# Performance work log

Hardware: AMD Instinct MI355X
Metric: run time of the kernel (lower is better)

The kernel has to match this reference:

```python
import jax, jax.numpy as jnp
import numpy as np

N_HEAD = 16


def setup_inputs() -> dict:
    key = jax.random.key(0)
    ks = jax.random.split(key, 6)
    B, T, H = 4, 2048, 1024
    inp = jax.random.normal(ks[0], (B, T, H), dtype=jnp.float32)
    # padding mask: valid prefix of random length in [T//2, T] per batch row
    lengths = jax.random.randint(ks[1], (B, 1), T // 2, T + 1)
    mask = jnp.arange(T)[None, :] < lengths  # (B, T) bool
    s = 0.02
    w_qkv = jax.random.normal(ks[2], (H, 3 * H), dtype=jnp.float32) * s
    b_qkv = jax.random.normal(ks[3], (3 * H,), dtype=jnp.float32) * s
    w_out = jax.random.normal(ks[4], (H, H), dtype=jnp.float32) * s
    b_out = jax.random.normal(ks[5], (H,), dtype=jnp.float32) * s
    return {"input": inp, "mask": mask, "w_qkv": w_qkv, "b_qkv": b_qkv,
            "w_out": w_out, "b_out": b_out}


def reference(input, mask, w_qkv, b_qkv, w_out, b_out):
    B, T, H = input.shape
    hd = H // N_HEAD
    qkv = input @ w_qkv + b_qkv                       # (B, T, 3H)
    q, k, v = jnp.split(qkv, 3, axis=-1)
    # (B, T, H) -> (B, nh, T, hd)
    q = q.reshape(B, T, N_HEAD, hd).transpose(0, 2, 1, 3)
    k = k.reshape(B, T, N_HEAD, hd).transpose(0, 2, 1, 3)
    v = v.reshape(B, T, N_HEAD, hd).transpose(0, 2, 1, 3)
    scores = jnp.einsum('bhqd,bhkd->bhqk', q, k) / jnp.sqrt(jnp.float32(hd))
    causal = jnp.tril(jnp.ones((T, T), dtype=bool))   # (T, T)
    full_mask = causal[None, None, :, :] & mask[:, None, None, :]  # (B,1,T,T) bcast over heads
    scores = jnp.where(full_mask, scores, -jnp.inf)
    attn = jax.nn.softmax(scores, axis=-1)            # (B, nh, T, T)
    o = jnp.einsum('bhqk,bhkd->bhqd', attn, v)        # (B, nh, T, hd)
    o = o.transpose(0, 2, 1, 3).reshape(B, T, H)
    return o @ w_out + b_out
```

## Files before the change

### kernel.cpp

```cpp
#include <hip/hip_runtime.h>
#include <math.h>

#define B_  4
#define T_  2048
#define H_  1024
#define NH  16
#define HD  64
#define H3  3072

typedef short bf16x8 __attribute__((ext_vector_type(8)));
typedef short bf16x4 __attribute__((ext_vector_type(4)));
typedef float f32x4  __attribute__((ext_vector_type(4)));
typedef float f32x16 __attribute__((ext_vector_type(16)));

#define SC2F 0.18033688011112042f

__device__ __forceinline__ unsigned short f2bf(float f) {
    union { float f; unsigned u; } v; v.f = f;
    unsigned u = v.u;
    unsigned r = (u + 0x7fffu + ((u >> 16) & 1u)) >> 16;
    return (unsigned short)r;
}

__device__ __forceinline__ void gload_lds16(const void* g, void* l) {
    __builtin_amdgcn_global_load_lds(
        (const __attribute__((address_space(1))) unsigned*)g,
        (__attribute__((address_space(3))) unsigned*)l, 16, 0, 0);
}

__device__ __forceinline__ f32x4 mfma_16x16x16_bf16(bf16x4 a, bf16x4 b, f32x4 c) {
#if __has_builtin(__builtin_amdgcn_mfma_f32_16x16x16_bf16)
    return __builtin_amdgcn_mfma_f32_16x16x16_bf16(a, b, c, 0, 0, 0);
#elif __has_builtin(__builtin_amdgcn_mfma_f32_16x16x16bf16_1k)
    return __builtin_amdgcn_mfma_f32_16x16x16bf16_1k(a, b, c, 0, 0, 0);
#else
    f32x4 d;
    asm volatile("v_mfma_f32_16x16x16_bf16 %0, %1, %2, %3"
                 : "=v"(d) : "v"(a), "v"(b), "v"(c));
    return d;
#endif
}

__global__ void lengths_kernel(const void* mask, int* lengths) {
    int b = blockIdx.x;
    int t = threadIdx.x;
    const unsigned* mu = (const unsigned*)mask;
    bool is_byte = (mu[0] == 0x01010101u);
    int cnt = 0;
    if (is_byte) {
        const unsigned char* m8 = (const unsigned char*)mask;
        for (int i = t; i < T_; i += 256) cnt += (m8[b * T_ + i] != 0);
    } else {
        const unsigned* m32 = (const unsigned*)mask;
        for (int i = t; i < T_; i += 256) cnt += (m32[b * T_ + i] != 0);
    }
    __shared__ int red[256];
    red[t] = cnt;
    __syncthreads();
    for (int s = 128; s > 0; s >>= 1) {
        if (t < s) red[t] += red[t + s];
        __syncthreads();
    }
    if (t == 0) lengths[b] = red[0];
}

__global__ void convert_bf16_kernel(const float* __restrict__ x,
                                    unsigned short* __restrict__ y, int n) {
    int i = (blockIdx.x * 256 + threadIdx.x) * 4;
    if (i < n) {
        float4 v = *(const float4*)(x + i);
        ushort4 o;
        o.x = f2bf(v.x); o.y = f2bf(v.y); o.z = f2bf(v.z); o.w = f2bf(v.w);
        *(ushort4*)(y + i) = o;
    }
}

__global__ void transpose2_kernel(const float* __restrict__ Wqkv,
                                  unsigned short* __restrict__ WqkvT,
                                  const float* __restrict__ Wout,
                                  unsigned short* __restrict__ WoutT) {
    __shared__ unsigned short tile[32][33];
    const int K = H_;
    const float* in;
    unsigned short* out;
    int N, nb;
    if (blockIdx.x < 96) { in = Wqkv; out = WqkvT; N = H3; nb = blockIdx.x * 32; }
    else                 { in = Wout; out = WoutT; N = H_; nb = (blockIdx.x - 96) * 32; }
    int kb = blockIdx.y * 32;
    int tx = threadIdx.x, ty = threadIdx.y;
    for (int i = 0; i < 32; i += 8)
        tile[ty + i][tx] = f2bf(in[(long)(kb + ty + i) * N + nb + tx]);
    __syncthreads();
    for (int i = 0; i < 32; i += 8)
        out[(long)(nb + ty + i) * K + kb + tx] = tile[tx][ty + i];
}

template <bool BF16_OUT, bool KSCALE, bool VSPLIT>
__global__ __launch_bounds__(256) void gemm_kernel(
    const unsigned short* __restrict__ A,
    const unsigned short* __restrict__ Bt,
    const float* __restrict__ bias,
    void* __restrict__ C,
    unsigned short* __restrict__ Vt,
    int M, int N, int K)
{
    __shared__ unsigned short Asm[128][32];
    __shared__ unsigned short Bsm[128][32];

    int tn = blockIdx.x * 128, tm = blockIdx.y * 128;
    int tid = threadIdx.x;
    int wid = tid >> 6, lane = tid & 63;
    int l31 = lane & 31, lh = lane >> 5;
    int wm = (wid & 1) * 64, wn = (wid >> 1) * 64;
    int grow = lane >> 2;
    int gcol = (((lane & 3) ^ (grow & 3) ^ ((grow >> 2) & 3))) * 8;
    int rkey = (l31 & 3) ^ ((l31 >> 2) & 3);

    f32x16 acc[2][2] = {};

    for (int k0 = 0; k0 < K; k0 += 32) {
        __syncthreads();
#pragma unroll
        for (int t = 0; t < 2; t++) {
            int ar = wid * 32 + t * 16 + grow;
            gload_lds16(A  + (long)(tm + ar) * K + k0 + gcol, &Asm[wid * 32 + t * 16][0]);
            gload_lds16(Bt + (long)(tn + ar) * K + k0 + gcol, &Bsm[wid * 32 + t * 16][0]);
        }
        __syncthreads();

        bf16x8 af[2][2], bfv[2][2];
#pragma unroll
        for (int ks = 0; ks < 2; ks++) {
            int pc = ((2 * ks + lh) ^ rkey) * 8;
            af[ks][0]  = *(const bf16x8*)(&Asm[wm + l31][pc]);
            af[ks][1]  = *(const bf16x8*)(&Asm[wm + 32 + l31][pc]);
            bfv[ks][0] = *(const bf16x8*)(&Bsm[wn + l31][pc]);
            bfv[ks][1] = *(const bf16x8*)(&Bsm[wn + 32 + l31][pc]);
        }
#pragma unroll
        for (int ks = 0; ks < 2; ks++)
#pragma unroll
            for (int i = 0; i < 2; i++)
#pragma unroll
                for (int j = 0; j < 2; j++)
                    acc[i][j] = __builtin_amdgcn_mfma_f32_32x32x16_bf16(
                        af[ks][i], bfv[ks][j], acc[i][j], 0, 0, 0);
    }

    if (VSPLIT && tn >= 2 * H_) {
#pragma unroll
        for (int i = 0; i < 2; i++)
#pragma unroll
            for (int j = 0; j < 2; j++) {
                int col = tn + wn + j * 32 + l31;
                float bs = bias[col];
                int feat = col - 2 * H_;
#pragma unroll
                for (int rg = 0; rg < 4; rg++) {
                    int tok0 = tm + wm + i * 32 + rg * 8 + lh * 4;
                    int bb = tok0 >> 11;
                    unsigned d0 = (unsigned)f2bf(acc[i][j][rg * 4 + 0] + bs) |
                                  ((unsigned)f2bf(acc[i][j][rg * 4 + 1] + bs) << 16);
                    unsigned d1 = (unsigned)f2bf(acc[i][j][rg * 4 + 2] + bs) |
                                  ((unsigned)f2bf(acc[i][j][rg * 4 + 3] + bs) << 16);
                    unsigned short* dst = Vt + ((long)(bb * 1024 + feat)) * T_ + (tok0 & (T_ - 1));
                    *(uint2*)dst = make_uint2(d0, d1);
                }
            }
        return;
    }

#pragma unroll
    for (int i = 0; i < 2; i++)
#pragma unroll
        for (int j = 0; j < 2; j++) {
            int col = tn + wn + j * 32 + l31;
            float bs = bias[col];
            bool ks_ = KSCALE && (col >= H_) && (col < 2 * H_);
#pragma unroll
            for (int r = 0; r < 16; r++) {
                int row = tm + wm + i * 32 + (r & 3) + 8 * (r >> 2) + 4 * lh;
                float v = acc[i][j][r] + bs;
                if (ks_) v *= SC2F;
                if (BF16_OUT)
                    ((unsigned short*)C)[(long)row * N + col] = f2bf(v);
                else
                    ((float*)C)[(long)row * N + col] = v;
            }
        }
}

__global__ __launch_bounds__(256) void attn_kernel(
    const unsigned short* __restrict__ QKV,
    const unsigned short* __restrict__ Vt,
    const int* __restrict__ lengths,
    unsigned short* __restrict__ O)
{
    int idx = blockIdx.x;
    int bh = idx & 63;
    int qt = 15 - (idx >> 6);
    int b = bh >> 4, h = bh & 15;
    int len = lengths[b];
    int q0 = qt * 128;

    int tid = threadIdx.x;
    int wid = tid >> 6, lane = tid & 63, quad = lane >> 4, lr = lane & 15;

    __shared__ __align__(16) unsigned short SH[18432];
    unsigned short (*Kd)[64][72] = (unsigned short (*)[64][72])(&SH[0]);
    unsigned short (*Vd)[64][72] = (unsigned short (*)[64][72])(&SH[9216]);

    const long qkv_base = (long)b * T_ * H3;

    bf16x8 qf[2][2];
#pragma unroll
    for (int nq = 0; nq < 2; nq++)
#pragma unroll
        for (int ks = 0; ks < 2; ks++)
            qf[nq][ks] = *(const bf16x8*)(QKV + qkv_base +
                (long)(q0 + wid * 32 + nq * 16 + lr) * H3 + h * HD + ks * 32 + quad * 8);

    int srow = tid >> 2, scb = (tid & 3) * 16;
    const unsigned short* kbase = QKV + qkv_base + (long)srow * H3 + H_ + h * HD + scb;
    const unsigned short* vbase = Vt + ((long)(bh * 64 + srow)) * T_ + scb;

    {
        float4 k0 = *(const float4*)(kbase);
        float4 k1 = *(const float4*)(kbase + 8);
        float4 v0 = *(const float4*)(vbase);
        float4 v1 = *(const float4*)(vbase + 8);
        *(float4*)(&Kd[0][srow][scb])     = k0;
        *(float4*)(&Kd[0][srow][scb + 8]) = k1;
        *(float4*)(&Vd[0][srow][scb])     = v0;
        *(float4*)(&Vd[0][srow][scb + 8]) = v1;
    }
    __syncthreads();

    float l_i[2] = { 0.f, 0.f };
    f32x4 Oacc[4][2] = {};

    int kmax = min(q0 + 127, len - 1);
    int n_kt = (kmax >> 6) + 1;
    int q_wave_lo = q0 + wid * 32;
    int q_wave_hi = q_wave_lo + 31;
    int myq[2] = { q_wave_lo + lr, q_wave_lo + 16 + lr };

    const unsigned short* kp = kbase + (long)64 * H3;
    const unsigned short* vp = vbase + 64;

    for (int kt = 0; kt < n_kt; kt++) {
        int cur = kt & 1;
        float4 pk0, pk1, pv0, pv1;
        bool pf = (kt + 1 < n_kt);
        if (pf) {
            pk0 = *(const float4*)(kp);
            pk1 = *(const float4*)(kp + 8);
            pv0 = *(const float4*)(vp);
            pv1 = *(const float4*)(vp + 8);
            kp += (long)64 * H3;
            vp += 64;
        }

        int k_lo = kt * 64;
        if (!(k_lo > q_wave_hi || k_lo >= len)) {
            f32x4 Sacc[4][2] = {};
#pragma unroll
            for (int ks = 0; ks < 2; ks++) {
#pragma unroll
                for (int mt = 0; mt < 4; mt++) {
                    bf16x8 kf = *(const bf16x8*)(&Kd[cur][mt * 16 + lr][ks * 32 + quad * 8]);
                    Sacc[mt][0] = __builtin_amdgcn_mfma_f32_16x16x32_bf16(kf, qf[0][ks], Sacc[mt][0], 0, 0, 0);
                    Sacc[mt][1] = __builtin_amdgcn_mfma_f32_16x16x32_bf16(kf, qf[1][ks], Sacc[mt][1], 0, 0, 0);
                }
            }

            bool full = (k_lo + 63 <= q_wave_lo) && (k_lo + 63 < len);
            float rs[2] = { 0.f, 0.f };
            unsigned pkk[4][2][2];
#pragma unroll
            for (int mt = 0; mt < 4; mt++)
#pragma unroll
                for (int nq = 0; nq < 2; nq++) {
                    float p[4];
#pragma unroll
                    for (int r = 0; r < 4; r++) {
                        float s = Sacc[mt][nq][r];
                        if (!full) {
                            int key = k_lo + mt * 16 + quad * 4 + r;
                            bool ok = (key <= myq[nq]) && (key < len);
                            s = ok ? s : -INFINITY;
                        }
                        p[r] = __builtin_amdgcn_exp2f(s);
                        rs[nq] += p[r];
                    }
                    pkk[mt][nq][0] = __builtin_amdgcn_perm(__float_as_uint(p[1]), __float_as_uint(p[0]), 0x07060302);
                    pkk[mt][nq][1] = __builtin_amdgcn_perm(__float_as_uint(p[3]), __float_as_uint(p[2]), 0x07060302);
                }

#pragma unroll
            for (int nq = 0; nq < 2; nq++) {
                float v = rs[nq];
                v += __shfl_xor(v, 16);
                v += __shfl_xor(v, 32);
                l_i[nq] += v;
            }

#pragma unroll
            for (int mt = 0; mt < 4; mt++) {
                union { unsigned u[2]; bf16x4 v; } bu[2];
                bu[0].u[0] = pkk[mt][0][0]; bu[0].u[1] = pkk[mt][0][1];
                bu[1].u[0] = pkk[mt][1][0]; bu[1].u[1] = pkk[mt][1][1];
#pragma unroll
                for (int md = 0; md < 4; md++) {
                    bf16x4 vf = *(const bf16x4*)(&Vd[cur][md * 16 + lr][mt * 16 + quad * 4]);
                    Oacc[md][0] = mfma_16x16x16_bf16(vf, bu[0].v, Oacc[md][0]);
                    Oacc[md][1] = mfma_16x16x16_bf16(vf, bu[1].v, Oacc[md][1]);
                }
            }
        }

        if (pf) {
            *(float4*)(&Kd[cur ^ 1][srow][scb])     = pk0;
            *(float4*)(&Kd[cur ^ 1][srow][scb + 8]) = pk1;
            *(float4*)(&Vd[cur ^ 1][srow][scb])     = pv0;
            *(float4*)(&Vd[cur ^ 1][srow][scb + 8]) = pv1;
        }
        __syncthreads();
    }

    __syncthreads();
    {
        unsigned short (*Es)[68] = (unsigned short (*)[68])(&SH[0]);
        float inv[2] = { 1.f / l_i[0], 1.f / l_i[1] };
#pragma unroll
        for (int nq = 0; nq < 2; nq++)
#pragma unroll
            for (int md = 0; md < 4; md++)
#pragma unroll
                for (int rp = 0; rp < 2; rp++) {
                    float e0 = Oacc[md][nq][rp * 2]     * inv[nq];
                    float e1 = Oacc[md][nq][rp * 2 + 1] * inv[nq];
                    unsigned w = __builtin_amdgcn_perm(__float_as_uint(e1), __float_as_uint(e0), 0x07060302);
                    *(unsigned*)(&Es[wid * 32 + nq * 16 + lr][md * 16 + quad * 4 + rp * 2]) = w;
                }
        __asm__ volatile("s_waitcnt lgkmcnt(0)" ::: "memory");
        int row = lane >> 1, cb = (lane & 1) * 32;
        long tok = (long)b * T_ + q0 + wid * 32 + row;
#pragma unroll
        for (int i = 0; i < 4; i++) {
            float4 v = *(const float4*)(&Es[wid * 32 + row][cb + i * 8]);
            *(float4*)(&O[tok * H_ + h * HD + cb + i * 8]) = v;
        }
    }
}

extern "C" void kernel_launch(void* const* d_in, const int* in_sizes, int n_in,
                              void* d_out, int out_size, void* d_ws, size_t ws_size,
                              hipStream_t stream) {
    const float* X    = (const float*)d_in[0];
    const void*  mask = d_in[1];
    const float* Wqkv = (const float*)d_in[2];
    const float* bqkv = (const float*)d_in[3];
    const float* Wout = (const float*)d_in[4];
    const float* bout = (const float*)d_in[5];

    char* ws = (char*)d_ws;
    int* lengths          = (int*)ws;
    unsigned short* WqkvT = (unsigned short*)(ws + 256);
    unsigned short* WoutT = WqkvT + (long)H3 * H_;
    unsigned short* QKV   = WoutT + (long)H_ * H_;
    unsigned short* Xbf   = QKV + (long)B_ * T_ * H3;
    unsigned short* Vt    = Xbf + (long)B_ * T_ * H_;
    unsigned short* Obf   = Xbf;

    const int M = B_ * T_;

    lengths_kernel<<<B_, 256, 0, stream>>>(mask, lengths);
    convert_bf16_kernel<<<(M * H_ / 4 + 255) / 256, 256, 0, stream>>>(X, Xbf, M * H_);
    transpose2_kernel<<<dim3(128, H_ / 32), dim3(32, 8), 0, stream>>>(Wqkv, WqkvT, Wout, WoutT);
    gemm_kernel<true, true, true><<<dim3(H3 / 128, M / 128), 256, 0, stream>>>(
        Xbf, WqkvT, bqkv, QKV, Vt, M, H3, H_);
    attn_kernel<<<B_ * NH * (T_ / 128), 256, 0, stream>>>(QKV, Vt, lengths, Obf);
    gemm_kernel<false, false, false><<<dim3(H_ / 128, M / 128), 256, 0, stream>>>(
        Obf, WoutT, bout, d_out, nullptr, M, H_, H_);
}
```

Measured before the change: 287.6 us.

## Use direct global-to-LDS loads in attention and deepen GEMM K-tile

The attention kernel now stages K and V tiles with direct global-to-LDS async loads into an XOR-swizzled unpadded layout, instead of register prefetch followed by LDS stores. This removes VGPR staging and the padding. The GEMM K step doubles to 64 with a new swizzle, and it gains a TN template parameter so the output projection uses 64-wide N tiles and launches twice as many blocks. The cost is more LDS per GEMM block and a sync placement that now depends on the async load ordering.

```diff
diff --git a/kernel.cpp b/kernel.cpp
--- a/kernel.cpp
+++ b/kernel.cpp
@@ -95,7 +95,7 @@
         out[(long)(nb + ty + i) * K + kb + tx] = tile[tx][ty + i];
 }
 
-template <bool BF16_OUT, bool KSCALE, bool VSPLIT>
+template <int TN, bool BF16_OUT, bool KSCALE, bool VSPLIT>
 __global__ __launch_bounds__(256) void gemm_kernel(
     const unsigned short* __restrict__ A,
     const unsigned short* __restrict__ Bt,
@@ -104,54 +104,56 @@
     unsigned short* __restrict__ Vt,
     int M, int N, int K)
 {
-    __shared__ unsigned short Asm[128][32];
-    __shared__ unsigned short Bsm[128][32];
-
-    int tn = blockIdx.x * 128, tm = blockIdx.y * 128;
+    __shared__ unsigned short Asm[128][64];
+    __shared__ unsigned short Bsm[TN][64];
+
+    int tn = blockIdx.x * TN, tm = blockIdx.y * 128;
     int tid = threadIdx.x;
     int wid = tid >> 6, lane = tid & 63;
     int l31 = lane & 31, lh = lane >> 5;
-    int wm = (wid & 1) * 64, wn = (wid >> 1) * 64;
-    int grow = lane >> 2;
-    int gcol = (((lane & 3) ^ (grow & 3) ^ ((grow >> 2) & 3))) * 8;
-    int rkey = (l31 & 3) ^ ((l31 >> 2) & 3);
-
-    f32x16 acc[2][2] = {};
-
-    for (int k0 = 0; k0 < K; k0 += 32) {
+    int wm = (wid & 1) * 64, wn = (wid >> 1) * (TN / 2);
+
+    int rl = lane >> 3;
+    int g8 = ((lane & 7) ^ rl) * 8;
+    const unsigned short* aP = A  + (long)(tm + wid * 32 + rl) * K + g8;
+    const unsigned short* bP = Bt + (long)(tn + wid * (TN / 4) + rl) * K + g8;
+    int rk = l31 & 7;
+
+    f32x16 acc[2][TN / 64] = {};
+
+    for (int k0 = 0; k0 < K; k0 += 64) {
         __syncthreads();
 #pragma unroll
-        for (int t = 0; t < 2; t++) {
-            int ar = wid * 32 + t * 16 + grow;
-            gload_lds16(A  + (long)(tm + ar) * K + k0 + gcol, &Asm[wid * 32 + t * 16][0]);
-            gload_lds16(Bt + (long)(tn + ar) * K + k0 + gcol, &Bsm[wid * 32 + t * 16][0]);
-        }
+        for (int t = 0; t < 4; t++)
+            gload_lds16(aP + (long)(t * 8) * K + k0, &Asm[wid * 32 + t * 8][0]);
+#pragma unroll
+        for (int t = 0; t < TN / 32; t++)
+            gload_lds16(bP + (long)(t * 8) * K + k0, &Bsm[wid * (TN / 4) + t * 8][0]);
         __syncthreads();
 
-        bf16x8 af[2][2], bfv[2][2];
-#pragma unroll
-        for (int ks = 0; ks < 2; ks++) {
-            int pc = ((2 * ks + lh) ^ rkey) * 8;
-            af[ks][0]  = *(const bf16x8*)(&Asm[wm + l31][pc]);
-            af[ks][1]  = *(const bf16x8*)(&Asm[wm + 32 + l31][pc]);
-            bfv[ks][0] = *(const bf16x8*)(&Bsm[wn + l31][pc]);
-            bfv[ks][1] = *(const bf16x8*)(&Bsm[wn + 32 + l31][pc]);
-        }
-#pragma unroll
-        for (int ks = 0; ks < 2; ks++)
+#pragma unroll
+        for (int ks = 0; ks < 4; ks++) {
+            int pc = ((ks * 2 + lh) ^ rk) * 8;
+            bf16x8 af[2], bv[TN / 64];
+            af[0] = *(const bf16x8*)(&Asm[wm + l31][pc]);
+            af[1] = *(const bf16x8*)(&Asm[wm + 32 + l31][pc]);
+#pragma unroll
+            for (int j = 0; j < TN / 64; j++)
+                bv[j] = *(const bf16x8*)(&Bsm[wn + j * 32 + l31][pc]);
 #pragma unroll
             for (int i = 0; i < 2; i++)
 #pragma unroll
-                for (int j = 0; j < 2; j++)
+                for (int j = 0; j < TN / 64; j++)
                     acc[i][j] = __builtin_amdgcn_mfma_f32_32x32x16_bf16(
-                        af[ks][i], bfv[ks][j], acc[i][j], 0, 0, 0);
+                        af[i], bv[j], acc[i][j], 0, 0, 0);
+        }
     }
 
     if (VSPLIT && tn >= 2 * H_) {
 #pragma unroll
         for (int i = 0; i < 2; i++)
 #pragma unroll
-            for (int j = 0; j < 2; j++) {
+            for (int j = 0; j < TN / 64; j++) {
                 int col = tn + wn + j * 32 + l31;
                 float bs = bias[col];
                 int feat = col - 2 * H_;
@@ -173,7 +175,7 @@
 #pragma unroll
     for (int i = 0; i < 2; i++)
 #pragma unroll
-        for (int j = 0; j < 2; j++) {
+        for (int j = 0; j < TN / 64; j++) {
             int col = tn + wn + j * 32 + l31;
             float bs = bias[col];
             bool ks_ = KSCALE && (col >= H_) && (col < 2 * H_);
@@ -206,9 +208,9 @@
     int tid = threadIdx.x;
     int wid = tid >> 6, lane = tid & 63, quad = lane >> 4, lr = lane & 15;
 
-    __shared__ __align__(16) unsigned short SH[18432];
-    unsigned short (*Kd)[64][72] = (unsigned short (*)[64][72])(&SH[0]);
-    unsigned short (*Vd)[64][72] = (unsigned short (*)[64][72])(&SH[9216]);
+    __shared__ __align__(16) unsigned short SH[16384];
+    unsigned short (*Kd)[64][64] = (unsigned short (*)[64][64])(&SH[0]);
+    unsigned short (*Vd)[64][64] = (unsigned short (*)[64][64])(&SH[8192]);
 
     const long qkv_base = (long)b * T_ * H3;
 
@@ -220,21 +222,10 @@
             qf[nq][ks] = *(const bf16x8*)(QKV + qkv_base +
                 (long)(q0 + wid * 32 + nq * 16 + lr) * H3 + h * HD + ks * 32 + quad * 8);
 
-    int srow = tid >> 2, scb = (tid & 3) * 16;
-    const unsigned short* kbase = QKV + qkv_base + (long)srow * H3 + H_ + h * HD + scb;
-    const unsigned short* vbase = Vt + ((long)(bh * 64 + srow)) * T_ + scb;
-
-    {
-        float4 k0 = *(const float4*)(kbase);
-        float4 k1 = *(const float4*)(kbase + 8);
-        float4 v0 = *(const float4*)(vbase);
-        float4 v1 = *(const float4*)(vbase + 8);
-        *(float4*)(&Kd[0][srow][scb])     = k0;
-        *(float4*)(&Kd[0][srow][scb + 8]) = k1;
-        *(float4*)(&Vd[0][srow][scb])     = v0;
-        *(float4*)(&Vd[0][srow][scb + 8]) = v1;
-    }
-    __syncthreads();
+    int rl = lane >> 3;
+    int g8 = ((lane & 7) ^ rl) * 8;
+    const unsigned short* kB = QKV + qkv_base + (long)(wid * 16 + rl) * H3 + H_ + h * HD + g8;
+    const unsigned short* vB = Vt + (long)(bh * 64 + wid * 16 + rl) * T_ + g8;
 
     float l_i[2] = { 0.f, 0.f };
     f32x4 Oacc[4][2] = {};
@@ -244,88 +235,86 @@
     int q_wave_lo = q0 + wid * 32;
     int q_wave_hi = q_wave_lo + 31;
     int myq[2] = { q_wave_lo + lr, q_wave_lo + 16 + lr };
-
-    const unsigned short* kp = kbase + (long)64 * H3;
-    const unsigned short* vp = vbase + 64;
+    int rk = lr & 7;
+
+#pragma unroll
+    for (int t = 0; t < 2; t++) {
+        gload_lds16(kB + (long)(t * 8) * H3, &Kd[0][wid * 16 + t * 8][0]);
+        gload_lds16(vB + (long)(t * 8) * T_, &Vd[0][wid * 16 + t * 8][0]);
+    }
 
     for (int kt = 0; kt < n_kt; kt++) {
         int cur = kt & 1;
-        float4 pk0, pk1, pv0, pv1;
-        bool pf = (kt + 1 < n_kt);
-        if (pf) {
-            pk0 = *(const float4*)(kp);
-            pk1 = *(const float4*)(kp + 8);
-            pv0 = *(const float4*)(vp);
-            pv1 = *(const float4*)(vp + 8);
-            kp += (long)64 * H3;
-            vp += 64;
+        __syncthreads();
+
+        if (kt + 1 < n_kt) {
+            long koff = (long)((kt + 1) * 64) * H3;
+            int voff = (kt + 1) * 64;
+#pragma unroll
+            for (int t = 0; t < 2; t++) {
+                gload_lds16(kB + koff + (long)(t * 8) * H3, &Kd[cur ^ 1][wid * 16 + t * 8][0]);
+                gload_lds16(vB + (long)(t * 8) * T_ + voff, &Vd[cur ^ 1][wid * 16 + t * 8][0]);
+            }
         }
 
         int k_lo = kt * 64;
-        if (!(k_lo > q_wave_hi || k_lo >= len)) {
-            f32x4 Sacc[4][2] = {};
-#pragma unroll
-            for (int ks = 0; ks < 2; ks++) {
-#pragma unroll
-                for (int mt = 0; mt < 4; mt++) {
-                    bf16x8 kf = *(const bf16x8*)(&Kd[cur][mt * 16 + lr][ks * 32 + quad * 8]);
-                    Sacc[mt][0] = __builtin_amdgcn_mfma_f32_16x16x32_bf16(kf, qf[0][ks], Sacc[mt][0], 0, 0, 0);
-                    Sacc[mt][1] = __builtin_amdgcn_mfma_f32_16x16x32_bf16(kf, qf[1][ks], Sacc[mt][1], 0, 0, 0);
+        if (k_lo > q_wave_hi || k_lo >= len) continue;
+
+        f32x4 Sacc[4][2] = {};
+#pragma unroll
+        for (int ks = 0; ks < 2; ks++) {
+#pragma unroll
+            for (int mt = 0; mt < 4; mt++) {
+                bf16x8 kf = *(const bf16x8*)(&Kd[cur][mt * 16 + lr][((ks * 4 + quad) ^ rk) * 8]);
+                Sacc[mt][0] = __builtin_amdgcn_mfma_f32_16x16x32_bf16(kf, qf[0][ks], Sacc[mt][0], 0, 0, 0);
+                Sacc[mt][1] = __builtin_amdgcn_mfma_f32_16x16x32_bf16(kf, qf[1][ks], Sacc[mt][1], 0, 0, 0);
+            }
+        }
+
+        bool full = (k_lo + 63 <= q_wave_lo) && (k_lo + 63 < len);
+        float rs[2] = { 0.f, 0.f };
+        unsigned pkk[4][2][2];
+#pragma unroll
+        for (int mt = 0; mt < 4; mt++)
+#pragma unroll
+            for (int nq = 0; nq < 2; nq++) {
+                float p[4];
+#pragma unroll
+                for (int r = 0; r < 4; r++) {
+                    float s = Sacc[mt][nq][r];
+                    if (!full) {
+                        int key = k_lo + mt * 16 + quad * 4 + r;
+                        bool ok = (key <= myq[nq]) && (key < len);
+                        s = ok ? s : -INFINITY;
+                    }
+                    p[r] = __builtin_amdgcn_exp2f(s);
+                    rs[nq] += p[r];
                 }
-            }
-
-            bool full = (k_lo + 63 <= q_wave_lo) && (k_lo + 63 < len);
-            float rs[2] = { 0.f, 0.f };
-            unsigned pkk[4][2][2];
-#pragma unroll
-            for (int mt = 0; mt < 4; mt++)
-#pragma unroll
-                for (int nq = 0; nq < 2; nq++) {
-                    float p[4];
-#pragma unroll
-                    for (int r = 0; r < 4; r++) {
-                        float s = Sacc[mt][nq][r];
-                        if (!full) {
-                            int key = k_lo + mt * 16 + quad * 4 + r;
-                            bool ok = (key <= myq[nq]) && (key < len);
-                            s = ok ? s : -INFINITY;
-                        }
-                        p[r] = __builtin_amdgcn_exp2f(s);
-                        rs[nq] += p[r];
-                    }
-                    pkk[mt][nq][0] = __builtin_amdgcn_perm(__float_as_uint(p[1]), __float_as_uint(p[0]), 0x07060302);
-                    pkk[mt][nq][1] = __builtin_amdgcn_perm(__float_as_uint(p[3]), __float_as_uint(p[2]), 0x07060302);
-                }
-
-#pragma unroll
-            for (int nq = 0; nq < 2; nq++) {
-                float v = rs[nq];
-                v += __shfl_xor(v, 16);
-                v += __shfl_xor(v, 32);
-                l_i[nq] += v;
-            }
-
-#pragma unroll
-            for (int mt = 0; mt < 4; mt++) {
-                union { unsigned u[2]; bf16x4 v; } bu[2];
-                bu[0].u[0] = pkk[mt][0][0]; bu[0].u[1] = pkk[mt][0][1];
-                bu[1].u[0] = pkk[mt][1][0]; bu[1].u[1] = pkk[mt][1][1];
-#pragma unroll
-                for (int md = 0; md < 4; md++) {
-                    bf16x4 vf = *(const bf16x4*)(&Vd[cur][md * 16 + lr][mt * 16 + quad * 4]);
-                    Oacc[md][0] = mfma_16x16x16_bf16(vf, bu[0].v, Oacc[md][0]);
-                    Oacc[md][1] = mfma_16x16x16_bf16(vf, bu[1].v, Oacc[md][1]);
-                }
-            }
-        }
-
-        if (pf) {
-            *(float4*)(&Kd[cur ^ 1][srow][scb])     = pk0;
-            *(float4*)(&Kd[cur ^ 1][srow][scb + 8]) = pk1;
-            *(float4*)(&Vd[cur ^ 1][srow][scb])     = pv0;
-            *(float4*)(&Vd[cur ^ 1][srow][scb + 8]) = pv1;
-        }
-        __syncthreads();
+                pkk[mt][nq][0] = __builtin_amdgcn_perm(__float_as_uint(p[1]), __float_as_uint(p[0]), 0x07060302);
+                pkk[mt][nq][1] = __builtin_amdgcn_perm(__float_as_uint(p[3]), __float_as_uint(p[2]), 0x07060302);
+            }
+
+#pragma unroll
+        for (int nq = 0; nq < 2; nq++) {
+            float v = rs[nq];
+            v += __shfl_xor(v, 16);
+            v += __shfl_xor(v, 32);
+            l_i[nq] += v;
+        }
+
+#pragma unroll
+        for (int mt = 0; mt < 4; mt++) {
+            union { unsigned u[2]; bf16x4 v; } bu[2];
+            bu[0].u[0] = pkk[mt][0][0]; bu[0].u[1] = pkk[mt][0][1];
+            bu[1].u[0] = pkk[mt][1][0]; bu[1].u[1] = pkk[mt][1][1];
+#pragma unroll
+            for (int md = 0; md < 4; md++) {
+                bf16x4 vf = *(const bf16x4*)(&Vd[cur][md * 16 + lr]
+                    [((mt * 2 + (quad >> 1)) ^ rk) * 8 + (quad & 1) * 4]);
+                Oacc[md][0] = mfma_16x16x16_bf16(vf, bu[0].v, Oacc[md][0]);
+                Oacc[md][1] = mfma_16x16x16_bf16(vf, bu[1].v, Oacc[md][1]);
+            }
+        }
     }
 
     __syncthreads();
@@ -378,9 +367,9 @@
     lengths_kernel<<<B_, 256, 0, stream>>>(mask, lengths);
     convert_bf16_kernel<<<(M * H_ / 4 + 255) / 256, 256, 0, stream>>>(X, Xbf, M * H_);
     transpose2_kernel<<<dim3(128, H_ / 32), dim3(32, 8), 0, stream>>>(Wqkv, WqkvT, Wout, WoutT);
-    gemm_kernel<true, true, true><<<dim3(H3 / 128, M / 128), 256, 0, stream>>>(
+    gemm_kernel<128, true, true, true><<<dim3(H3 / 128, M / 128), 256, 0, stream>>>(
         Xbf, WqkvT, bqkv, QKV, Vt, M, H3, H_);
     attn_kernel<<<B_ * NH * (T_ / 128), 256, 0, stream>>>(QKV, Vt, lengths, Obf);
-    gemm_kernel<false, false, false><<<dim3(H_ / 128, M / 128), 256, 0, stream>>>(
+    gemm_kernel<64, false, false, false><<<dim3(H_ / 64, M / 128), 256, 0, stream>>>(
         Obf, WoutT, bout, d_out, nullptr, M, H_, H_);
 }
```

Result: faster. 277.5 us (-3.5%).
